# Kernel tuning notes

Hardware: AMD Instinct MI355X
Metric: run time of the kernel (lower is better)

## Reference

```python
import jax, jax.numpy as jnp
import numpy as np

B = 64
FEATS = [96, 64, 64, 64]   # per-level input features
NCNT = [1, 8, 64, 512]     # per-level node counts
NODES = 512                # nodes at current depth (tree[-1])
DEG = 8                    # branching degree at this depth
IN_F = 64                  # features[depth]
OUT_F = 64                 # features[depth+1]
SUP = 640                  # in_f * 10 support hidden


def setup_inputs() -> dict:
    key = jax.random.key(0)
    ks = jax.random.split(key, 12)
    inp = {}
    for i in range(4):
        inp[f"x{i}"] = jax.random.normal(ks[i], (B, NCNT[i], FEATS[i]), jnp.float32)
        inp[f"W{i}"] = jax.random.normal(ks[4 + i], (FEATS[i], OUT_F), jnp.float32) / np.sqrt(FEATS[i]).astype(np.float32)
    inp["branch"] = jax.random.normal(ks[8], (NODES, IN_F, IN_F * DEG), jnp.float32) / np.float32(8.0)
    inp["Ws1"] = jax.random.normal(ks[9], (IN_F, SUP), jnp.float32) / np.float32(8.0)
    inp["Ws2"] = jax.random.normal(ks[10], (SUP, OUT_F), jnp.float32) / np.sqrt(SUP).astype(np.float32)
    bound = np.float32(1.0 / np.sqrt(OUT_F))
    inp["bias"] = jax.random.uniform(ks[11], (1, DEG, OUT_F), jnp.float32, -bound, bound)
    return inp


def _lrelu(v):
    return jnp.where(v > 0, v, 0.2 * v)


def reference(x0, x1, x2, x3, W0, W1, W2, W3, branch, Ws1, Ws2, bias):
    xs = [x0, x1, x2, x3]
    Ws = [W0, W1, W2, W3]
    # multi-depth linear sum: project each ancestor level, replicate each
    # node's vector contiguously down to `NODES` rows (torch repeat+view)
    y = jnp.zeros((B, NODES, OUT_F), jnp.float32)
    for x, W in zip(xs, Ws):
        t = x @ W                                   # (B, n_i, OUT_F)
        y = y + jnp.repeat(t, NODES // t.shape[1], axis=1)
    # branching: per-node weight slice (GEMV per node, shared over batch)
    xb = _lrelu(jnp.einsum('bnf,nfg->bng', x3, branch))  # (B, NODES, IN_F*DEG)
    xb = xb.reshape(B, NODES * DEG, IN_F)
    xb = (xb @ Ws1) @ Ws2                           # support MLP -> (B, NODES*DEG, OUT_F)
    y = xb + jnp.repeat(y, DEG, axis=1)             # y repeat(1,1,deg).view
    y = _lrelu(y + jnp.tile(bias, (1, NODES, 1)))   # bias.repeat(1, nodes, 1)
    return y
```

## Files before the change

kernel.cpp:

```cpp
#include <hip/hip_runtime.h>


typedef float f32x4 __attribute__((ext_vector_type(4)));
typedef __bf16 bf16x8 __attribute__((ext_vector_type(8)));

__device__ __forceinline__ unsigned short f2bf(float f) {
    union { float f; unsigned int u; } x; x.f = f;
    unsigned int r = x.u + 0x7FFFu + ((x.u >> 16) & 1u);
    return (unsigned short)(r >> 16);
}

__global__ __launch_bounds__(256) void tree_prep(
    const float* __restrict__ x0, const float* __restrict__ W0,
    const float* __restrict__ x1, const float* __restrict__ W1,
    const float* __restrict__ x2, const float* __restrict__ W2,
    const float* __restrict__ x3, const float* __restrict__ W3,
    const float* __restrict__ Ws1, const float* __restrict__ Ws2,
    float* __restrict__ ylg, unsigned short* __restrict__ xbf,
    unsigned short* __restrict__ wsF, unsigned short* __restrict__ w3f)
{
    const int t = threadIdx.x;
    const int blk = blockIdx.x;
    if (blk < 1024) {
        __shared__ float red[4][64];
        const int b = blk >> 4, q = blk & 15;
        const int f = t & 63, kq = t >> 6;
        float p0 = 0.f, p1 = 0.f;
        const float* x0p = x0 + b * 96 + kq * 24;
        #pragma unroll 6
        for (int k = 0; k < 24; k += 2) {
            p0 += x0p[k]     * W0[(kq * 24 + k) * 64 + f];
            p1 += x0p[k + 1] * W0[(kq * 24 + k + 1) * 64 + f];
        }
        const int oct = q >> 1;
        const float* x1p = x1 + b * 512 + oct * 64 + kq * 16;
        #pragma unroll 8
        for (int k = 0; k < 16; k += 2) {
            p0 += x1p[k]     * W1[(kq * 16 + k) * 64 + f];
            p1 += x1p[k + 1] * W1[(kq * 16 + k + 1) * 64 + f];
        }
        red[kq][f] = p0 + p1;
        __syncthreads();
        const int gl = t >> 6;
        const int g = q * 4 + gl;
        float acc = red[0][f] + red[1][f] + red[2][f] + red[3][f];
        const float* x2p = x2 + (size_t)b * 4096 + g * 64;
        float c0 = 0.f, c1 = 0.f;
        #pragma unroll 8
        for (int k = 0; k < 64; k += 2) {
            c0 += x2p[k]     * W2[k * 64 + f];
            c1 += x2p[k + 1] * W2[(k + 1) * 64 + f];
        }
        acc += c0 + c1;
        const int mt = b >> 4, l4m = (b >> 2) & 3, rm = b & 3;
        const int ft = f >> 4, l15 = f & 15;
        ylg[(size_t)((g * 4 + mt) * 4 + ft) * 256 + (l4m * 16 + l15) * 4 + rm] = acc;
    } else if (blk < 1536) {
        const int bb = blk - 1024;
        const int b = bb >> 3, q = bb & 7;
        const int n = q * 64 + (t >> 2), kq = t & 3;
        const int mt = b >> 4, l15b = b & 15;
        const float* src = x3 + (size_t)b * 32768 + (size_t)n * 64 + kq * 16;
        #pragma unroll
        for (int i = 0; i < 4; ++i) {
            float4 v = *(const float4*)(src + 4 * i);
            const int k0 = kq * 16 + 4 * i;
            const int ks = k0 >> 5, l4k = (k0 >> 3) & 3, j = k0 & 7;
            union { unsigned short h[4]; uint2 u; } p;
            p.h[0] = f2bf(v.x); p.h[1] = f2bf(v.y); p.h[2] = f2bf(v.z); p.h[3] = f2bf(v.w);
            *(uint2*)&xbf[(size_t)n * 4096 +
                          ((mt * 2 + ks) * 64 + l4k * 16 + l15b) * 8 + j] = p.u;
        }
    } else if (blk < 1600) {
        __shared__ float red[4][64];
        const int c = blk - 1536;
        const int f = t & 63, q = t >> 6;
        const float* w1p = Ws1 + (size_t)c * 640 + q * 160;
        const float* w2p = Ws2 + (size_t)(q * 160) * 64 + f;
        float a0 = 0.f, a1 = 0.f;
        #pragma unroll 8
        for (int s = 0; s < 160; s += 2) {
            a0 += w1p[s]     * w2p[(size_t)s * 64];
            a1 += w1p[s + 1] * w2p[(size_t)(s + 1) * 64];
        }
        red[q][f] = a0 + a1;
        __syncthreads();
        if (q == 0) {
            const float v = red[0][f] + red[1][f] + red[2][f] + red[3][f];
            const int ks = c >> 5, l4c = (c >> 3) & 3, j = c & 7;
            wsF[((f >> 4) * 2 + ks) * 512 + (l4c * 16 + (f & 15)) * 8 + j] = f2bf(v);
        }
    } else {
        const int l = t & 63;
        #pragma unroll
        for (int it = 0; it < 2; ++it) {
            const int fh = it * 4 + (t >> 6);
            const int ft = fh >> 1, ks = fh & 1;
            const int f = ft * 16 + (l & 15);
            const int kb = ks * 32 + (l >> 4) * 8;
            union { unsigned short h[8]; uint4 u; } p;
            #pragma unroll
            for (int j = 0; j < 8; ++j) p.h[j] = f2bf(W3[(kb + j) * 64 + f]);
            *(uint4*)&w3f[((size_t)fh * 64 + l) * 8] = p.u;
        }
    }
}

__global__ __launch_bounds__(256, 4) void tree_main(
    const float* __restrict__ branch, const float* __restrict__ bias,
    const float* __restrict__ ylg, const unsigned short* __restrict__ xbf,
    const unsigned short* __restrict__ wsF, const unsigned short* __restrict__ w3f,
    float* __restrict__ out)
{
    __shared__ unsigned short mem[64 * 258];
    const int t = threadIdx.x;
    const int w = t >> 6, l = t & 63;
    const int l15 = l & 15, l4 = l >> 4;
    const int blk = (blockIdx.x & 7) * 128 + (blockIdx.x >> 3);
    const int n = blk >> 1, dh = blk & 1;
    const int d = 4 * dh + w;
    const int g = n >> 3;

    bf16x8 bx[4][2];
    #pragma unroll
    for (int bt = 0; bt < 4; ++bt)
        #pragma unroll
        for (int ks = 0; ks < 2; ++ks)
            bx[bt][ks] = *(const bf16x8*)(xbf + (size_t)n * 4096 +
                                          ((bt * 2 + ks) * 64 + l) * 8);

    {
        const float* bp = branch + (size_t)n * 32768 + dh * 256;
        #pragma unroll
        for (int half = 0; half < 2; ++half) {
            f32x4 stg[8];
            #pragma unroll
            for (int i = 0; i < 8; ++i) {
                const int fi = (half * 8 + i) * 256 + t;
                const int k = fi >> 6, c4 = (fi & 63) << 2;
                stg[i] = *(const f32x4*)(bp + (size_t)k * 512 + c4);
            }
            #pragma unroll
            for (int i = 0; i < 8; ++i) {
                const int fi = (half * 8 + i) * 256 + t;
                const int k = fi >> 6, c4 = (fi & 63) << 2;
                union { unsigned short h[4]; uint2 u; } q;
                q.h[0] = f2bf(stg[i][0]); q.h[1] = f2bf(stg[i][1]);
                q.h[2] = f2bf(stg[i][2]); q.h[3] = f2bf(stg[i][3]);
                *(uint2*)&mem[k * 258 + c4] = q.u;
            }
        }
    }
    __syncthreads();

    bf16x8 pf[4][2];
    #pragma unroll
    for (int cP = 0; cP < 4; ++cP)
        #pragma unroll
        for (int ks = 0; ks < 2; ++ks) {
            union { unsigned short h[8]; bf16x8 bv; } p;
            #pragma unroll
            for (int j = 0; j < 8; ++j)
                p.h[j] = mem[(32 * ks + 8 * l4 + j) * 258 + w * 64 + 16 * cP + l15];
            pf[cP][ks] = p.bv;
        }
    __syncthreads();

    unsigned short* ts = mem + w * (16 * 72);

    float* outp = out + (size_t)(n * 8 + d) * 64;
    #pragma unroll
    for (int bt = 0; bt < 4; ++bt) {
        #pragma unroll
        for (int cP = 0; cP < 4; ++cP) {
            f32x4 s = {0.f, 0.f, 0.f, 0.f};
            s = __builtin_amdgcn_mfma_f32_16x16x32_bf16(pf[cP][0], bx[bt][0], s, 0, 0, 0);
            s = __builtin_amdgcn_mfma_f32_16x16x32_bf16(pf[cP][1], bx[bt][1], s, 0, 0, 0);
            union { unsigned short h[4]; uint2 u; } q;
            #pragma unroll
            for (int r = 0; r < 4; ++r) {
                float v = s[r];
                v = fmaxf(v, 0.2f * v);
                q.h[r] = f2bf(v);
            }
            *(uint2*)&ts[l15 * 72 + 16 * cP + 4 * l4] = q.u;
        }
        bf16x8 a20 = *(const bf16x8*)&ts[l15 * 72 + 8 * l4];
        bf16x8 a21 = *(const bf16x8*)&ts[l15 * 72 + 32 + 8 * l4];
        #pragma unroll
        for (int ft = 0; ft < 4; ++ft) {
            f32x4 o = *(const f32x4*)(ylg + (size_t)((g * 4 + bt) * 4 + ft) * 256 + l * 4);
            bf16x8 w30 = *(const bf16x8*)(w3f + (size_t)((ft * 2 + 0) * 64 + l) * 8);
            bf16x8 w31 = *(const bf16x8*)(w3f + (size_t)((ft * 2 + 1) * 64 + l) * 8);
            bf16x8 wf0 = *(const bf16x8*)(wsF + (size_t)((ft * 2 + 0) * 64 + l) * 8);
            bf16x8 wf1 = *(const bf16x8*)(wsF + (size_t)((ft * 2 + 1) * 64 + l) * 8);
            o = __builtin_amdgcn_mfma_f32_16x16x32_bf16(bx[bt][0], w30, o, 0, 0, 0);
            o = __builtin_amdgcn_mfma_f32_16x16x32_bf16(bx[bt][1], w31, o, 0, 0, 0);
            o = __builtin_amdgcn_mfma_f32_16x16x32_bf16(a20, wf0, o, 0, 0, 0);
            o = __builtin_amdgcn_mfma_f32_16x16x32_bf16(a21, wf1, o, 0, 0, 0);
            const float bv = bias[d * 64 + 16 * ft + l15];
            #pragma unroll
            for (int r = 0; r < 4; ++r) {
                float val = o[r] + bv;
                val = fmaxf(val, 0.2f * val);
                outp[(size_t)(16 * bt + 4 * l4 + r) * 262144 + 16 * ft + l15] = val;
            }
        }
    }
}

extern "C" void kernel_launch(void* const* d_in, const int* in_sizes, int n_in,
                              void* d_out, int out_size, void* d_ws, size_t ws_size,
                              hipStream_t stream) {
    (void)in_sizes; (void)n_in; (void)out_size; (void)ws_size;
    const float* x0     = (const float*)d_in[0];
    const float* W0     = (const float*)d_in[1];
    const float* x1     = (const float*)d_in[2];
    const float* W1     = (const float*)d_in[3];
    const float* x2     = (const float*)d_in[4];
    const float* W2     = (const float*)d_in[5];
    const float* x3     = (const float*)d_in[6];
    const float* W3     = (const float*)d_in[7];
    const float* branch = (const float*)d_in[8];
    const float* Ws1    = (const float*)d_in[9];
    const float* Ws2    = (const float*)d_in[10];
    const float* bias   = (const float*)d_in[11];

    float* ylg          = (float*)d_ws;
    unsigned short* xbf = (unsigned short*)((char*)d_ws + 1048576);
    unsigned short* wsF = (unsigned short*)((char*)d_ws + 5242880);
    unsigned short* w3f = (unsigned short*)((char*)d_ws + 5251072);
    float* out = (float*)d_out;

    tree_prep<<<1601, 256, 0, stream>>>(x0, W0, x1, W1, x2, W2, x3, W3, Ws1, Ws2,
                                        ylg, xbf, wsF, w3f);
    tree_main<<<1024, 256, 0, stream>>>(branch, bias, ylg, xbf, wsF, w3f, out);
}
```

Baseline: 43.98 us.

## Process both degree halves per block with prefetched second branch slab

Each block now handles one node and both halves of its degree dimension, so the grid is halved. The second half of the branch weight slab is loaded into registers before the first half is computed, hiding its global-memory latency behind the first half's MFMA work. The xbf fragments are loaded once per node instead of twice. The cost is more LDS per block (two slabs plus separate scratch), 16-entry register staging, and fewer resident blocks (launch bound lowered to 2), which may reduce occupancy-based latency hiding.

```diff
diff --git a/kernel.cpp b/kernel.cpp
--- a/kernel.cpp
+++ b/kernel.cpp
@@ -106,20 +106,20 @@
     }
 }
 
-__global__ __launch_bounds__(256, 4) void tree_main(
+__global__ __launch_bounds__(256, 2) void tree_main(
     const float* __restrict__ branch, const float* __restrict__ bias,
     const float* __restrict__ ylg, const unsigned short* __restrict__ xbf,
     const unsigned short* __restrict__ wsF, const unsigned short* __restrict__ w3f,
     float* __restrict__ out)
 {
-    __shared__ unsigned short mem[64 * 258];
+    __shared__ unsigned short brB[2][64 * 258];
+    __shared__ unsigned short tsb[4][16 * 72];
     const int t = threadIdx.x;
     const int w = t >> 6, l = t & 63;
     const int l15 = l & 15, l4 = l >> 4;
-    const int blk = (blockIdx.x & 7) * 128 + (blockIdx.x >> 3);
-    const int n = blk >> 1, dh = blk & 1;
-    const int d = 4 * dh + w;
+    const int n = (blockIdx.x & 7) * 64 + (blockIdx.x >> 3);
     const int g = n >> 3;
+    unsigned short* ts = tsb[w];
 
     bf16x8 bx[4][2];
     #pragma unroll
@@ -130,83 +130,106 @@
                                           ((bt * 2 + ks) * 64 + l) * 8);
 
     {
-        const float* bp = branch + (size_t)n * 32768 + dh * 256;
-        #pragma unroll
-        for (int half = 0; half < 2; ++half) {
-            f32x4 stg[8];
-            #pragma unroll
-            for (int i = 0; i < 8; ++i) {
-                const int fi = (half * 8 + i) * 256 + t;
-                const int k = fi >> 6, c4 = (fi & 63) << 2;
-                stg[i] = *(const f32x4*)(bp + (size_t)k * 512 + c4);
+        const float* bp = branch + (size_t)n * 32768;
+        f32x4 stg[16];
+        #pragma unroll
+        for (int i = 0; i < 16; ++i) {
+            const int fi = i * 256 + t;
+            const int k = fi >> 6, c4 = (fi & 63) << 2;
+            stg[i] = *(const f32x4*)(bp + (size_t)k * 512 + c4);
+        }
+        #pragma unroll
+        for (int i = 0; i < 16; ++i) {
+            const int fi = i * 256 + t;
+            const int k = fi >> 6, c4 = (fi & 63) << 2;
+            union { unsigned short h[4]; uint2 u; } q;
+            q.h[0] = f2bf(stg[i][0]); q.h[1] = f2bf(stg[i][1]);
+            q.h[2] = f2bf(stg[i][2]); q.h[3] = f2bf(stg[i][3]);
+            *(uint2*)&brB[0][k * 258 + c4] = q.u;
+        }
+    }
+    __syncthreads();
+
+    f32x4 stg1[16];
+    {
+        const float* bp = branch + (size_t)n * 32768 + 256;
+        #pragma unroll
+        for (int i = 0; i < 16; ++i) {
+            const int fi = i * 256 + t;
+            const int k = fi >> 6, c4 = (fi & 63) << 2;
+            stg1[i] = *(const f32x4*)(bp + (size_t)k * 512 + c4);
+        }
+    }
+
+    auto compute = [&](const unsigned short* br, const int d) {
+        bf16x8 pf[4][2];
+        #pragma unroll
+        for (int cP = 0; cP < 4; ++cP)
+            #pragma unroll
+            for (int ks = 0; ks < 2; ++ks) {
+                union { unsigned short h[8]; bf16x8 bv; } p;
+                #pragma unroll
+                for (int j = 0; j < 8; ++j)
+                    p.h[j] = br[(32 * ks + 8 * l4 + j) * 258 + w * 64 + 16 * cP + l15];
+                pf[cP][ks] = p.bv;
             }
-            #pragma unroll
-            for (int i = 0; i < 8; ++i) {
-                const int fi = (half * 8 + i) * 256 + t;
-                const int k = fi >> 6, c4 = (fi & 63) << 2;
+        float* outp = out + (size_t)(n * 8 + d) * 64;
+        #pragma unroll
+        for (int bt = 0; bt < 4; ++bt) {
+            #pragma unroll
+            for (int cP = 0; cP < 4; ++cP) {
+                f32x4 s = {0.f, 0.f, 0.f, 0.f};
+                s = __builtin_amdgcn_mfma_f32_16x16x32_bf16(pf[cP][0], bx[bt][0], s, 0, 0, 0);
+                s = __builtin_amdgcn_mfma_f32_16x16x32_bf16(pf[cP][1], bx[bt][1], s, 0, 0, 0);
                 union { unsigned short h[4]; uint2 u; } q;
-                q.h[0] = f2bf(stg[i][0]); q.h[1] = f2bf(stg[i][1]);
-                q.h[2] = f2bf(stg[i][2]); q.h[3] = f2bf(stg[i][3]);
-                *(uint2*)&mem[k * 258 + c4] = q.u;
+                #pragma unroll
+                for (int r = 0; r < 4; ++r) {
+                    float v = s[r];
+                    v = fmaxf(v, 0.2f * v);
+                    q.h[r] = f2bf(v);
+                }
+                *(uint2*)&ts[l15 * 72 + 16 * cP + 4 * l4] = q.u;
             }
+            bf16x8 a20 = *(const bf16x8*)&ts[l15 * 72 + 8 * l4];
+            bf16x8 a21 = *(const bf16x8*)&ts[l15 * 72 + 32 + 8 * l4];
+            #pragma unroll
+            for (int ft = 0; ft < 4; ++ft) {
+                f32x4 o = *(const f32x4*)(ylg + (size_t)((g * 4 + bt) * 4 + ft) * 256 + l * 4);
+                bf16x8 w30 = *(const bf16x8*)(w3f + (size_t)((ft * 2 + 0) * 64 + l) * 8);
+                bf16x8 w31 = *(const bf16x8*)(w3f + (size_t)((ft * 2 + 1) * 64 + l) * 8);
+                bf16x8 wf0 = *(const bf16x8*)(wsF + (size_t)((ft * 2 + 0) * 64 + l) * 8);
+                bf16x8 wf1 = *(const bf16x8*)(wsF + (size_t)((ft * 2 + 1) * 64 + l) * 8);
+                o = __builtin_amdgcn_mfma_f32_16x16x32_bf16(bx[bt][0], w30, o, 0, 0, 0);
+                o = __builtin_amdgcn_mfma_f32_16x16x32_bf16(bx[bt][1], w31, o, 0, 0, 0);
+                o = __builtin_amdgcn_mfma_f32_16x16x32_bf16(a20, wf0, o, 0, 0, 0);
+                o = __builtin_amdgcn_mfma_f32_16x16x32_bf16(a21, wf1, o, 0, 0, 0);
+                const float bv = bias[d * 64 + 16 * ft + l15];
+                #pragma unroll
+                for (int r = 0; r < 4; ++r) {
+                    float val = o[r] + bv;
+                    val = fmaxf(val, 0.2f * val);
+                    outp[(size_t)(16 * bt + 4 * l4 + r) * 262144 + 16 * ft + l15] = val;
+                }
+            }
+        }
+    };
+
+    compute(brB[0], w);
+
+    {
+        #pragma unroll
+        for (int i = 0; i < 16; ++i) {
+            const int fi = i * 256 + t;
+            const int k = fi >> 6, c4 = (fi & 63) << 2;
+            union { unsigned short h[4]; uint2 u; } q;
+            q.h[0] = f2bf(stg1[i][0]); q.h[1] = f2bf(stg1[i][1]);
+            q.h[2] = f2bf(stg1[i][2]); q.h[3] = f2bf(stg1[i][3]);
+            *(uint2*)&brB[1][k * 258 + c4] = q.u;
         }
     }
     __syncthreads();
 
-    bf16x8 pf[4][2];
-    #pragma unroll
-    for (int cP = 0; cP < 4; ++cP)
-        #pragma unroll
-        for (int ks = 0; ks < 2; ++ks) {
-            union { unsigned short h[8]; bf16x8 bv; } p;
-            #pragma unroll
-            for (int j = 0; j < 8; ++j)
-                p.h[j] = mem[(32 * ks + 8 * l4 + j) * 258 + w * 64 + 16 * cP + l15];
-            pf[cP][ks] = p.bv;
-        }
-    __syncthreads();
-
-    unsigned short* ts = mem + w * (16 * 72);
-
-    float* outp = out + (size_t)(n * 8 + d) * 64;
-    #pragma unroll
-    for (int bt = 0; bt < 4; ++bt) {
-        #pragma unroll
-        for (int cP = 0; cP < 4; ++cP) {
-            f32x4 s = {0.f, 0.f, 0.f, 0.f};
-            s = __builtin_amdgcn_mfma_f32_16x16x32_bf16(pf[cP][0], bx[bt][0], s, 0, 0, 0);
-            s = __builtin_amdgcn_mfma_f32_16x16x32_bf16(pf[cP][1], bx[bt][1], s, 0, 0, 0);
-            union { unsigned short h[4]; uint2 u; } q;
-            #pragma unroll
-            for (int r = 0; r < 4; ++r) {
-                float v = s[r];
-                v = fmaxf(v, 0.2f * v);
-                q.h[r] = f2bf(v);
-            }
-            *(uint2*)&ts[l15 * 72 + 16 * cP + 4 * l4] = q.u;
-        }
-        bf16x8 a20 = *(const bf16x8*)&ts[l15 * 72 + 8 * l4];
-        bf16x8 a21 = *(const bf16x8*)&ts[l15 * 72 + 32 + 8 * l4];
-        #pragma unroll
-        for (int ft = 0; ft < 4; ++ft) {
-            f32x4 o = *(const f32x4*)(ylg + (size_t)((g * 4 + bt) * 4 + ft) * 256 + l * 4);
-            bf16x8 w30 = *(const bf16x8*)(w3f + (size_t)((ft * 2 + 0) * 64 + l) * 8);
-            bf16x8 w31 = *(const bf16x8*)(w3f + (size_t)((ft * 2 + 1) * 64 + l) * 8);
-            bf16x8 wf0 = *(const bf16x8*)(wsF + (size_t)((ft * 2 + 0) * 64 + l) * 8);
-            bf16x8 wf1 = *(const bf16x8*)(wsF + (size_t)((ft * 2 + 1) * 64 + l) * 8);
-            o = __builtin_amdgcn_mfma_f32_16x16x32_bf16(bx[bt][0], w30, o, 0, 0, 0);
-            o = __builtin_amdgcn_mfma_f32_16x16x32_bf16(bx[bt][1], w31, o, 0, 0, 0);
-            o = __builtin_amdgcn_mfma_f32_16x16x32_bf16(a20, wf0, o, 0, 0, 0);
-            o = __builtin_amdgcn_mfma_f32_16x16x32_bf16(a21, wf1, o, 0, 0, 0);
-            const float bv = bias[d * 64 + 16 * ft + l15];
-            #pragma unroll
-            for (int r = 0; r < 4; ++r) {
-                float val = o[r] + bv;
-                val = fmaxf(val, 0.2f * val);
-                outp[(size_t)(16 * bt + 4 * l4 + r) * 262144 + 16 * ft + l15] = val;
-            }
-        }
-    }
+    compute(brB[1], 4 + w);
 }
 
 extern "C" void kernel_launch(void* const* d_in, const int* in_sizes, int n_in,
@@ -234,5 +257,5 @@
 
     tree_prep<<<1601, 256, 0, stream>>>(x0, W0, x1, W1, x2, W2, x3, W3, Ws1, Ws2,
                                         ylg, xbf, wsF, w3f);
-    tree_main<<<1024, 256, 0, stream>>>(branch, bias, ylg, xbf, wsF, w3f, out);
-}
+    tree_main<<<512, 256, 0, stream>>>(branch, bias, ylg, xbf, wsF, w3f, out);
+}
```

Result: slower. 49.69 us (+13.0%).

## Split main kernel per (node, degree) block with one batch tile per wave

Applied to the files above, without the earlier changes.

Remaps tree_main so that each block handles a single node-degree pair and each wave handles one batch tile, rather than each block handling four degrees across all four batch tiles. The grid grows fourfold, shared memory shrinks to a 64x64 branch slice plus per-wave scratch, and one __syncthreads is removed. Launch bounds rise to 6 waves per SIMD to raise occupancy and latency hiding. In exchange, the xbf and weight fragments are reloaded by more blocks, and branch loads become narrower 256-byte row segments.

```diff
diff --git a/kernel.cpp b/kernel.cpp
--- a/kernel.cpp
+++ b/kernel.cpp
@@ -106,49 +106,43 @@
     }
 }
 
-__global__ __launch_bounds__(256, 4) void tree_main(
+__global__ __launch_bounds__(256, 6) void tree_main(
     const float* __restrict__ branch, const float* __restrict__ bias,
     const float* __restrict__ ylg, const unsigned short* __restrict__ xbf,
     const unsigned short* __restrict__ wsF, const unsigned short* __restrict__ w3f,
     float* __restrict__ out)
 {
-    __shared__ unsigned short mem[64 * 258];
+    __shared__ unsigned short brB[64 * 68];
+    __shared__ unsigned short tsb[4][16 * 72];
     const int t = threadIdx.x;
     const int w = t >> 6, l = t & 63;
     const int l15 = l & 15, l4 = l >> 4;
-    const int blk = (blockIdx.x & 7) * 128 + (blockIdx.x >> 3);
-    const int n = blk >> 1, dh = blk & 1;
-    const int d = 4 * dh + w;
+    const int blk = (blockIdx.x & 7) * 512 + (blockIdx.x >> 3);
+    const int n = blk >> 3, d = blk & 7;
     const int g = n >> 3;
-
-    bf16x8 bx[4][2];
-    #pragma unroll
-    for (int bt = 0; bt < 4; ++bt)
-        #pragma unroll
-        for (int ks = 0; ks < 2; ++ks)
-            bx[bt][ks] = *(const bf16x8*)(xbf + (size_t)n * 4096 +
-                                          ((bt * 2 + ks) * 64 + l) * 8);
+    const int bt = w;
+    unsigned short* ts = tsb[w];
+
+    bf16x8 bx0 = *(const bf16x8*)(xbf + (size_t)n * 4096 + ((bt * 2 + 0) * 64 + l) * 8);
+    bf16x8 bx1 = *(const bf16x8*)(xbf + (size_t)n * 4096 + ((bt * 2 + 1) * 64 + l) * 8);
 
     {
-        const float* bp = branch + (size_t)n * 32768 + dh * 256;
-        #pragma unroll
-        for (int half = 0; half < 2; ++half) {
-            f32x4 stg[8];
-            #pragma unroll
-            for (int i = 0; i < 8; ++i) {
-                const int fi = (half * 8 + i) * 256 + t;
-                const int k = fi >> 6, c4 = (fi & 63) << 2;
-                stg[i] = *(const f32x4*)(bp + (size_t)k * 512 + c4);
-            }
-            #pragma unroll
-            for (int i = 0; i < 8; ++i) {
-                const int fi = (half * 8 + i) * 256 + t;
-                const int k = fi >> 6, c4 = (fi & 63) << 2;
-                union { unsigned short h[4]; uint2 u; } q;
-                q.h[0] = f2bf(stg[i][0]); q.h[1] = f2bf(stg[i][1]);
-                q.h[2] = f2bf(stg[i][2]); q.h[3] = f2bf(stg[i][3]);
-                *(uint2*)&mem[k * 258 + c4] = q.u;
-            }
+        const float* bp = branch + (size_t)n * 32768 + d * 64;
+        f32x4 stg[4];
+        #pragma unroll
+        for (int i = 0; i < 4; ++i) {
+            const int fi = i * 256 + t;
+            const int k = fi >> 4, c4 = (fi & 15) << 2;
+            stg[i] = *(const f32x4*)(bp + (size_t)k * 512 + c4);
+        }
+        #pragma unroll
+        for (int i = 0; i < 4; ++i) {
+            const int fi = i * 256 + t;
+            const int k = fi >> 4, c4 = (fi & 15) << 2;
+            union { unsigned short h[4]; uint2 u; } q;
+            q.h[0] = f2bf(stg[i][0]); q.h[1] = f2bf(stg[i][1]);
+            q.h[2] = f2bf(stg[i][2]); q.h[3] = f2bf(stg[i][3]);
+            *(uint2*)&brB[k * 68 + c4] = q.u;
         }
     }
     __syncthreads();
@@ -161,50 +155,44 @@
             union { unsigned short h[8]; bf16x8 bv; } p;
             #pragma unroll
             for (int j = 0; j < 8; ++j)
-                p.h[j] = mem[(32 * ks + 8 * l4 + j) * 258 + w * 64 + 16 * cP + l15];
+                p.h[j] = brB[(32 * ks + 8 * l4 + j) * 68 + 16 * cP + l15];
             pf[cP][ks] = p.bv;
         }
-    __syncthreads();
-
-    unsigned short* ts = mem + w * (16 * 72);
 
     float* outp = out + (size_t)(n * 8 + d) * 64;
     #pragma unroll
-    for (int bt = 0; bt < 4; ++bt) {
-        #pragma unroll
-        for (int cP = 0; cP < 4; ++cP) {
-            f32x4 s = {0.f, 0.f, 0.f, 0.f};
-            s = __builtin_amdgcn_mfma_f32_16x16x32_bf16(pf[cP][0], bx[bt][0], s, 0, 0, 0);
-            s = __builtin_amdgcn_mfma_f32_16x16x32_bf16(pf[cP][1], bx[bt][1], s, 0, 0, 0);
-            union { unsigned short h[4]; uint2 u; } q;
-            #pragma unroll
-            for (int r = 0; r < 4; ++r) {
-                float v = s[r];
-                v = fmaxf(v, 0.2f * v);
-                q.h[r] = f2bf(v);
-            }
-            *(uint2*)&ts[l15 * 72 + 16 * cP + 4 * l4] = q.u;
-        }
-        bf16x8 a20 = *(const bf16x8*)&ts[l15 * 72 + 8 * l4];
-        bf16x8 a21 = *(const bf16x8*)&ts[l15 * 72 + 32 + 8 * l4];
-        #pragma unroll
-        for (int ft = 0; ft < 4; ++ft) {
-            f32x4 o = *(const f32x4*)(ylg + (size_t)((g * 4 + bt) * 4 + ft) * 256 + l * 4);
-            bf16x8 w30 = *(const bf16x8*)(w3f + (size_t)((ft * 2 + 0) * 64 + l) * 8);
-            bf16x8 w31 = *(const bf16x8*)(w3f + (size_t)((ft * 2 + 1) * 64 + l) * 8);
-            bf16x8 wf0 = *(const bf16x8*)(wsF + (size_t)((ft * 2 + 0) * 64 + l) * 8);
-            bf16x8 wf1 = *(const bf16x8*)(wsF + (size_t)((ft * 2 + 1) * 64 + l) * 8);
-            o = __builtin_amdgcn_mfma_f32_16x16x32_bf16(bx[bt][0], w30, o, 0, 0, 0);
-            o = __builtin_amdgcn_mfma_f32_16x16x32_bf16(bx[bt][1], w31, o, 0, 0, 0);
-            o = __builtin_amdgcn_mfma_f32_16x16x32_bf16(a20, wf0, o, 0, 0, 0);
-            o = __builtin_amdgcn_mfma_f32_16x16x32_bf16(a21, wf1, o, 0, 0, 0);
-            const float bv = bias[d * 64 + 16 * ft + l15];
-            #pragma unroll
-            for (int r = 0; r < 4; ++r) {
-                float val = o[r] + bv;
-                val = fmaxf(val, 0.2f * val);
-                outp[(size_t)(16 * bt + 4 * l4 + r) * 262144 + 16 * ft + l15] = val;
-            }
+    for (int cP = 0; cP < 4; ++cP) {
+        f32x4 s = {0.f, 0.f, 0.f, 0.f};
+        s = __builtin_amdgcn_mfma_f32_16x16x32_bf16(pf[cP][0], bx0, s, 0, 0, 0);
+        s = __builtin_amdgcn_mfma_f32_16x16x32_bf16(pf[cP][1], bx1, s, 0, 0, 0);
+        union { unsigned short h[4]; uint2 u; } q;
+        #pragma unroll
+        for (int r = 0; r < 4; ++r) {
+            float v = s[r];
+            v = fmaxf(v, 0.2f * v);
+            q.h[r] = f2bf(v);
+        }
+        *(uint2*)&ts[l15 * 72 + 16 * cP + 4 * l4] = q.u;
+    }
+    bf16x8 a20 = *(const bf16x8*)&ts[l15 * 72 + 8 * l4];
+    bf16x8 a21 = *(const bf16x8*)&ts[l15 * 72 + 32 + 8 * l4];
+    #pragma unroll
+    for (int ft = 0; ft < 4; ++ft) {
+        f32x4 o = *(const f32x4*)(ylg + (size_t)((g * 4 + bt) * 4 + ft) * 256 + l * 4);
+        bf16x8 w30 = *(const bf16x8*)(w3f + (size_t)((ft * 2 + 0) * 64 + l) * 8);
+        bf16x8 w31 = *(const bf16x8*)(w3f + (size_t)((ft * 2 + 1) * 64 + l) * 8);
+        bf16x8 wf0 = *(const bf16x8*)(wsF + (size_t)((ft * 2 + 0) * 64 + l) * 8);
+        bf16x8 wf1 = *(const bf16x8*)(wsF + (size_t)((ft * 2 + 1) * 64 + l) * 8);
+        o = __builtin_amdgcn_mfma_f32_16x16x32_bf16(bx0, w30, o, 0, 0, 0);
+        o = __builtin_amdgcn_mfma_f32_16x16x32_bf16(bx1, w31, o, 0, 0, 0);
+        o = __builtin_amdgcn_mfma_f32_16x16x32_bf16(a20, wf0, o, 0, 0, 0);
+        o = __builtin_amdgcn_mfma_f32_16x16x32_bf16(a21, wf1, o, 0, 0, 0);
+        const float bv = bias[d * 64 + 16 * ft + l15];
+        #pragma unroll
+        for (int r = 0; r < 4; ++r) {
+            float val = o[r] + bv;
+            val = fmaxf(val, 0.2f * val);
+            outp[(size_t)(16 * bt + 4 * l4 + r) * 262144 + 16 * ft + l15] = val;
         }
     }
 }
@@ -234,5 +222,5 @@
 
     tree_prep<<<1601, 256, 0, stream>>>(x0, W0, x1, W1, x2, W2, x3, W3, Ws1, Ws2,
                                         ylg, xbf, wsF, w3f);
-    tree_main<<<1024, 256, 0, stream>>>(branch, bias, ylg, xbf, wsF, w3f, out);
-}
+    tree_main<<<4096, 256, 0, stream>>>(branch, bias, ylg, xbf, wsF, w3f, out);
+}
```

Measured after the change: 43.67 us. About the same (-0.7%).
